# Kernel optimization log

Hardware: AMD Instinct MI355X
Metric: run time of the kernel (lower is better)

The kernel has to match this reference:

```python
import jax, jax.numpy as jnp
import numpy as np

TEMPERATURE = 0.05
BETA = 1.0
LAMBDA_THRESHOLD = 0.7


def setup_inputs() -> dict:
    key = jax.random.key(0)
    k1, k2 = jax.random.split(key)
    B, D = 8192, 256
    features = jax.random.normal(k1, (B, D), dtype=jnp.float32)
    labels = jax.random.randint(k2, (B,), 0, 100, dtype=jnp.int64)
    return {"features": features, "labels": labels}


def reference(features, labels):
    B = features.shape[0]
    eps = 1e-12
    # L2 normalize rows
    f = features / jnp.maximum(jnp.linalg.norm(features, axis=1, keepdims=True), eps)
    sim = jnp.matmul(f, f.T) / TEMPERATURE                      # [B, B]
    sim_max = jnp.max(sim, axis=1, keepdims=True)               # [B, 1]
    sim_stable = sim - sim_max

    same = (labels[:, None] == labels[None, :])
    eye = jnp.eye(B, dtype=bool)
    pos_mask = same & ~eye                                       # [B, B] bool

    # Denominator: logsumexp over all non-self entries per row
    exp_sim = jnp.exp(sim_stable) * (~eye)
    log_denom = jnp.log(jnp.sum(exp_sim, axis=1, keepdims=True) + eps) + sim_max  # [B,1]

    # SCL term: mean over positive pairs of (log_denom[i] - sim[i,j])
    pos_f = pos_mask.astype(sim.dtype)
    n_pos = jnp.sum(pos_f)
    scl_sum = jnp.sum(pos_f * (log_denom - sim))
    scl_loss = jnp.where(n_pos > 0, scl_sum / jnp.maximum(n_pos, 1.0), 0.0)

    # Relaxation term: per row, logsumexp over high-sim positive logits + baseline
    high = (sim * TEMPERATURE > LAMBDA_THRESHOLD) & pos_mask     # [B, B] bool
    neg_inf = jnp.asarray(-jnp.inf, sim.dtype)
    masked_logits = jnp.where(high, sim_stable, neg_inf)          # [B, B]
    baseline = (1.0 / TEMPERATURE) - sim_max                      # [B, 1]
    all_logits = jnp.concatenate([masked_logits, baseline], axis=1)  # [B, B+1]
    row_lse = jax.nn.logsumexp(all_logits, axis=1)                # [B]
    row_has = jnp.any(high, axis=1)
    n_high = jnp.sum(high.astype(sim.dtype))
    relax_sum = jnp.sum(jnp.where(row_has, row_lse, 0.0))
    relaxation_loss = jnp.where(n_high > 0, relax_sum / jnp.maximum(n_high, 1.0), 0.0)

    total = scl_loss + BETA * relaxation_loss
    return jnp.clip(total, 0.0, 10.0)
```

## Files before the change

kernel.cpp:

```cpp
#include <hip/hip_runtime.h>
#include <hip/hip_bf16.h>
#include <math.h>

#define B_N 8192
#define D_K 256
#define TILE 128
#define NT 512
#define NBLK 64
#define NPAIR 2080
#define NCLS 100
#define KEXP 28.8539008177792681f

typedef __attribute__((ext_vector_type(8))) short short8;
typedef __attribute__((ext_vector_type(4))) float f32x4;

__device__ __forceinline__ unsigned short f2bf(float x) {
    unsigned int u = __float_as_uint(x);
    unsigned int r = (u + 0x7FFFu + ((u >> 16) & 1u)) >> 16;
    return (unsigned short)r;
}

__device__ __forceinline__ void gload_lds16(const short* g, short* l) {
    __builtin_amdgcn_global_load_lds(
        (const __attribute__((address_space(1))) void*)g,
        (__attribute__((address_space(3))) void*)l, 16, 0, 0);
}

__device__ __forceinline__ float row_sum16(float v) {
    v += __int_as_float(__builtin_amdgcn_update_dpp(0, __float_as_int(v), 0xB1, 0xF, 0xF, true));
    v += __int_as_float(__builtin_amdgcn_update_dpp(0, __float_as_int(v), 0x4E, 0xF, 0xF, true));
    v += __int_as_float(__builtin_amdgcn_update_dpp(0, __float_as_int(v), 0x141, 0xF, 0xF, true));
    v += __int_as_float(__builtin_amdgcn_update_dpp(0, __float_as_int(v), 0x140, 0xF, 0xF, true));
    return v;
}

__global__ void prep_kernel(const float* __restrict__ feat, unsigned short* __restrict__ fnorm,
                            const int* __restrict__ labels, int* __restrict__ cnt,
                            float* __restrict__ gscal, double* __restrict__ accum,
                            unsigned int* __restrict__ done) {
    if (blockIdx.x == 0) {
        __shared__ int h[NCLS];
        int t = threadIdx.x;
        if (t < NCLS) h[t] = 0;
        if (t == 0) {
            gscal[0] = 0.f; gscal[1] = 0.f;
            accum[0] = 0.0; accum[1] = 0.0; accum[2] = 0.0;
            *done = 0u;
        }
        __syncthreads();
        for (int r = t; r < B_N; r += 256) atomicAdd(&h[labels[r]], 1);
        __syncthreads();
        if (t < NCLS) cnt[t] = h[t];
    }
    int wave = threadIdx.x >> 6, lane = threadIdx.x & 63;
    int row = blockIdx.x * 4 + wave;
    float4 v = *(const float4*)(feat + (size_t)row * D_K + lane * 4);
    float ss = v.x * v.x + v.y * v.y + v.z * v.z + v.w * v.w;
    #pragma unroll
    for (int off = 1; off < 64; off <<= 1) ss += __shfl_xor(ss, off);
    float inv = 1.0f / fmaxf(sqrtf(ss), 1e-12f);
    ushort4 o;
    o.x = f2bf(v.x * inv); o.y = f2bf(v.y * inv);
    o.z = f2bf(v.z * inv); o.w = f2bf(v.w * inv);
    *(ushort4*)(fnorm + (size_t)row * D_K + lane * 4) = o;
}

__global__ __launch_bounds__(NT, 4) void main_kernel(
        const unsigned short* __restrict__ fnorm, const int* __restrict__ labels,
        float2* __restrict__ G, float* __restrict__ gscal) {
    int bid = blockIdx.x;
    int b = (int)((sqrtf(8.0f * bid + 1.0f) - 1.0f) * 0.5f);
    while ((b + 1) * (b + 2) / 2 <= bid) ++b;
    while (b * (b + 1) / 2 > bid) --b;
    int a = bid - b * (b + 1) / 2;
    const int row0 = a * TILE, col0 = b * TILE;
    const bool diag = (a == b);

    __shared__ short As[2][TILE * 64];
    __shared__ short Bs[2][TILE * 64];
    __shared__ int Ls[2 * TILE];
    __shared__ int ghs[8];
    __shared__ float gps[8];

    const int tid = threadIdx.x;
    const int lane = tid & 63, wave = tid >> 6;
    const int wm = wave >> 2, wn = wave & 3;
    const int l15 = lane & 15, lhi = lane >> 4;
    const short* fn = (const short*)fnorm;

    const int id0 = tid, id1 = tid + NT;
    const int r0s = id0 >> 3, c0s = (id0 & 7) ^ (r0s & 7), u0 = (id0 & ~63) * 8;
    const int r1s = id1 >> 3, c1s = (id1 & 7) ^ (r1s & 7), u1 = (id1 & ~63) * 8;

    if (tid < 128) Ls[tid] = labels[row0 + tid];
    else if (tid < 256) Ls[tid] = labels[col0 + tid - 128];
    if (lane == 0) ghs[wave] = 0;

    {
        gload_lds16(fn + (size_t)(row0 + r0s) * D_K + c0s * 8, &As[0][u0]);
        gload_lds16(fn + (size_t)(row0 + r1s) * D_K + c1s * 8, &As[0][u1]);
        if (!diag) {
            gload_lds16(fn + (size_t)(col0 + r0s) * D_K + c0s * 8, &Bs[0][u0]);
            gload_lds16(fn + (size_t)(col0 + r1s) * D_K + c1s * 8, &Bs[0][u1]);
        }
    }

    f32x4 acc[4][2];
    #pragma unroll
    for (int i = 0; i < 4; i++)
        #pragma unroll
        for (int j = 0; j < 2; j++) acc[i][j] = {0.f, 0.f, 0.f, 0.f};

    #pragma unroll
    for (int kc = 0; kc < 4; ++kc) {
        const int cur = kc & 1;
        __syncthreads();
        if (kc < 3) {
            const int nxt = cur ^ 1, ko = (kc + 1) * 64;
            gload_lds16(fn + (size_t)(row0 + r0s) * D_K + ko + c0s * 8, &As[nxt][u0]);
            gload_lds16(fn + (size_t)(row0 + r1s) * D_K + ko + c1s * 8, &As[nxt][u1]);
            if (!diag) {
                gload_lds16(fn + (size_t)(col0 + r0s) * D_K + ko + c0s * 8, &Bs[nxt][u0]);
                gload_lds16(fn + (size_t)(col0 + r1s) * D_K + ko + c1s * 8, &Bs[nxt][u1]);
            }
        }
        const short* Asrc = As[cur];
        const short* Bsrc = diag ? As[cur] : Bs[cur];
        #pragma unroll
        for (int ks = 0; ks < 2; ++ks) {
            short8 af[4], bfr[2];
            #pragma unroll
            for (int mi = 0; mi < 4; mi++) {
                int row = wm * 64 + mi * 16 + l15;
                int ch = (ks * 4 + lhi) ^ (l15 & 7);
                af[mi] = *(const short8*)&Asrc[row * 64 + ch * 8];
            }
            #pragma unroll
            for (int ni = 0; ni < 2; ni++) {
                int row = wn * 32 + ni * 16 + l15;
                int ch = (ks * 4 + lhi) ^ (l15 & 7);
                bfr[ni] = *(const short8*)&Bsrc[row * 64 + ch * 8];
            }
            #pragma unroll
            for (int mi = 0; mi < 4; mi++)
                #pragma unroll
                for (int ni = 0; ni < 2; ni++)
                    acc[mi][ni] = __builtin_amdgcn_mfma_f32_16x16x32_bf16(af[mi], bfr[ni], acc[mi][ni], 0, 0, 0);
        }
    }
    __syncthreads();

    float2* Rbuf = (float2*)As[0];
    float2* Cbuf = (float2*)Bs[0];

    int lc[2], colg[2];
    #pragma unroll
    for (int ni = 0; ni < 2; ni++) {
        int c = wn * 32 + ni * 16 + l15;
        lc[ni] = Ls[128 + c];
        colg[ni] = col0 + c;
    }

    float cD[2] = {0.f, 0.f};
    float gp = 0.f;
    unsigned int hmask = 0;

    #pragma unroll
    for (int mi = 0; mi < 4; mi++) {
        #pragma unroll
        for (int reg = 0; reg < 4; reg++) {
            int rloc = wm * 64 + mi * 16 + lhi * 4 + reg;
            int rowg = row0 + rloc;
            int lr = Ls[rloc];
            float d = 0.f;
            #pragma unroll
            for (int ni = 0; ni < 2; ni++) {
                float dot = acc[mi][ni][reg];
                float e = __builtin_exp2f((dot - 1.0f) * KEXP);
                bool ns = (rowg != colg[ni]);
                float ev = ns ? e : 0.f;
                d += ev; cD[ni] += ev;
                bool ps = ns && (lr == lc[ni]);
                gp += ps ? dot : 0.f;
                bool hi = ps && (dot > 0.7f);
                hmask |= hi ? (1u << ((mi * 4 + reg) * 2 + ni)) : 0u;
            }
            d = row_sum16(d);
            if (l15 == 0) Rbuf[wn * 128 + rloc] = {d, 0.f};
        }
    }

    if (!diag) {
        #pragma unroll
        for (int ni = 0; ni < 2; ni++) {
            cD[ni] += __shfl_xor(cD[ni], 16);
            cD[ni] += __shfl_xor(cD[ni], 32);
        }
        if (lhi == 0) {
            #pragma unroll
            for (int ni = 0; ni < 2; ni++)
                Cbuf[wm * 128 + wn * 32 + ni * 16 + l15] = {cD[ni], 0.f};
        }
    }

    gp = row_sum16(gp);
    gp += __shfl_xor(gp, 16);
    gp += __shfl_xor(gp, 32);
    if (lane == 0) gps[wave] = gp;

    if (__any(hmask != 0)) {
        float cR[2] = {0.f, 0.f};
        #pragma unroll
        for (int mi = 0; mi < 4; mi++) {
            #pragma unroll
            for (int reg = 0; reg < 4; reg++) {
                int rloc = wm * 64 + mi * 16 + lhi * 4 + reg;
                float rx = 0.f;
                #pragma unroll
                for (int ni = 0; ni < 2; ni++) {
                    if (hmask & (1u << ((mi * 4 + reg) * 2 + ni))) {
                        float e = __builtin_exp2f((acc[mi][ni][reg] - 1.0f) * KEXP);
                        rx += e; cR[ni] += e;
                    }
                }
                rx = row_sum16(rx);
                if (l15 == 0) Rbuf[wn * 128 + rloc].y = rx;
            }
        }
        if (!diag) {
            #pragma unroll
            for (int ni = 0; ni < 2; ni++) {
                cR[ni] += __shfl_xor(cR[ni], 16);
                cR[ni] += __shfl_xor(cR[ni], 32);
            }
            if (lhi == 0) {
                #pragma unroll
                for (int ni = 0; ni < 2; ni++)
                    Cbuf[wm * 128 + wn * 32 + ni * 16 + l15].y = cR[ni];
            }
        }
        int nhi = __popc(hmask);
        #pragma unroll
        for (int off = 1; off < 64; off <<= 1) nhi += __shfl_xor(nhi, off);
        if (lane == 0) ghs[wave] = nhi;
    }
    __syncthreads();

    if (tid < 128) {
        int r = tid;
        float2 a0 = Rbuf[r], a1 = Rbuf[128 + r], a2 = Rbuf[256 + r], a3 = Rbuf[384 + r];
        G[(size_t)b * B_N + row0 + r] = {a0.x + a1.x + a2.x + a3.x, a0.y + a1.y + a2.y + a3.y};
    } else if (tid < 256 && !diag) {
        int c = tid - 128;
        float2 a0 = Cbuf[c], a1 = Cbuf[128 + c];
        G[(size_t)a * B_N + col0 + c] = {a0.x + a1.x, a0.y + a1.y};
    }
    if (tid == 0) {
        float w = diag ? 1.0f : 2.0f;
        float gpt = gps[0] + gps[1] + gps[2] + gps[3] + gps[4] + gps[5] + gps[6] + gps[7];
        atomicAdd(&gscal[0], w * gpt);
        int tot = ghs[0] + ghs[1] + ghs[2] + ghs[3] + ghs[4] + ghs[5] + ghs[6] + ghs[7];
        if (tot > 0) atomicAdd(&gscal[1], w * (float)tot);
    }
}

__global__ void finalize_kernel(const float2* __restrict__ G, const int* __restrict__ labels,
                                const int* __restrict__ cnt, const float* __restrict__ gscal,
                                double* __restrict__ accum, unsigned int* __restrict__ done,
                                float* __restrict__ out) {
    int lane = threadIdx.x & 63, q = threadIdx.x >> 6;
    int r = blockIdx.x * 64 + lane;
    float d = 0.f, rx = 0.f;
    #pragma unroll
    for (int s = 0; s < 16; ++s) {
        float2 g = G[(size_t)(q * 16 + s) * B_N + r];
        d += g.x; rx += g.y;
    }
    __shared__ float2 sh[4][64];
    sh[q][lane] = {d, rx};
    __syncthreads();
    if (threadIdx.x < 64) {
        int rr = blockIdx.x * 64 + threadIdx.x;
        float2 t0 = sh[0][threadIdx.x], t1 = sh[1][threadIdx.x];
        float2 t2 = sh[2][threadIdx.x], t3 = sh[3][threadIdx.x];
        float dd = t0.x + t1.x + t2.x + t3.x;
        float rr2 = t0.y + t1.y + t2.y + t3.y;
        float np = (float)(cnt[labels[rr]] - 1);
        float ld = logf(dd + 1e-12f) + 20.0f;
        double s1 = (double)np * (double)ld;
        double s2 = (double)np;
        double s3 = (rr2 > 0.f) ? (double)logf(rr2 + 1.0f) : 0.0;
        #pragma unroll
        for (int off = 1; off < 64; off <<= 1) {
            s1 += __shfl_xor(s1, off);
            s2 += __shfl_xor(s2, off);
            s3 += __shfl_xor(s3, off);
        }
        if (threadIdx.x == 0) {
            atomicAdd(&accum[0], s1);
            atomicAdd(&accum[1], s2);
            atomicAdd(&accum[2], s3);
            __threadfence();
            unsigned int tk = atomicAdd(done, 1u);
            if (tk == gridDim.x - 1) {
                double a1 = atomicAdd(&accum[0], 0.0);
                double a2 = atomicAdd(&accum[1], 0.0);
                double a3 = atomicAdd(&accum[2], 0.0);
                double gp = (double)gscal[0];
                double gh = (double)gscal[1];
                double scl = (a2 > 0.0) ? (a1 - 20.0 * gp) / fmax(a2, 1.0) : 0.0;
                double rel = (gh > 0.0) ? a3 / fmax(gh, 1.0) : 0.0;
                double tot = scl + rel;
                tot = fmin(fmax(tot, 0.0), 10.0);
                out[0] = (float)tot;
            }
        }
    }
}

extern "C" void kernel_launch(void* const* d_in, const int* in_sizes, int n_in,
                              void* d_out, int out_size, void* d_ws, size_t ws_size,
                              hipStream_t stream) {
    const float* feat = (const float*)d_in[0];
    const int* labels = (const int*)d_in[1];
    float* out = (float*)d_out;
    char* ws = (char*)d_ws;

    unsigned short* fnorm = (unsigned short*)(ws);
    float2* G          = (float2*)(ws + (size_t)4 * 1024 * 1024);
    int*    cnt        = (int*)(ws + (size_t)8 * 1024 * 1024);
    float*  gscal      = (float*)(ws + (size_t)8 * 1024 * 1024 + 1024);
    double* accum      = (double*)(ws + (size_t)8 * 1024 * 1024 + 2048);
    unsigned int* done = (unsigned int*)(ws + (size_t)8 * 1024 * 1024 + 3072);

    prep_kernel<<<B_N / 4, 256, 0, stream>>>(feat, fnorm, labels, cnt, gscal, accum, done);
    main_kernel<<<NPAIR, NT, 0, stream>>>(fnorm, labels, G, gscal);
    finalize_kernel<<<B_N / 64, 256, 0, stream>>>(G, labels, cnt, gscal, accum, done, out);
    (void)in_sizes; (void)n_in; (void)out_size; (void)ws_size;
}
```

Before: 120.6 us.

## Halve K-chunk LDS tiles, raise occupancy, template epilogue on diagonal flag

Cuts the per-stage K chunk from 64 to 32 so each double-buffered LDS tile is half the size, with one async global-to-LDS load per thread per stage and precomputed swizzled fragment offsets. Launch bounds go from 4 to 8 blocks per SM to allow more resident blocks. The epilogue is specialised on a compile-time diagonal flag, and the high-similarity bitmask is replaced by recomputing the condition in the second pass. The aim is lower LDS and register pressure and higher occupancy, at the cost of twice as many barrier-separated pipeline stages and a tighter register budget that may cause spills.

```diff
diff --git a/kernel.cpp b/kernel.cpp
--- a/kernel.cpp
+++ b/kernel.cpp
@@ -10,9 +10,13 @@
 #define NPAIR 2080
 #define NCLS 100
 #define KEXP 28.8539008177792681f
+#define KCH 32
+#define NCHUNK 8
 
 typedef __attribute__((ext_vector_type(8))) short short8;
 typedef __attribute__((ext_vector_type(4))) float f32x4;
+
+template <bool V> struct BoolC { static constexpr bool value = V; };
 
 __device__ __forceinline__ unsigned short f2bf(float x) {
     unsigned int u = __float_as_uint(x);
@@ -65,7 +69,7 @@
     *(ushort4*)(fnorm + (size_t)row * D_K + lane * 4) = o;
 }
 
-__global__ __launch_bounds__(NT, 4) void main_kernel(
+__global__ __launch_bounds__(NT, 8) void main_kernel(
         const unsigned short* __restrict__ fnorm, const int* __restrict__ labels,
         float2* __restrict__ G, float* __restrict__ gscal) {
     int bid = blockIdx.x;
@@ -76,8 +80,8 @@
     const int row0 = a * TILE, col0 = b * TILE;
     const bool diag = (a == b);
 
-    __shared__ short As[2][TILE * 64];
-    __shared__ short Bs[2][TILE * 64];
+    __shared__ short As[2][TILE * KCH];
+    __shared__ short Bs[2][TILE * KCH];
     __shared__ int Ls[2 * TILE];
     __shared__ int ghs[8];
     __shared__ float gps[8];
@@ -88,22 +92,17 @@
     const int l15 = lane & 15, lhi = lane >> 4;
     const short* fn = (const short*)fnorm;
 
-    const int id0 = tid, id1 = tid + NT;
-    const int r0s = id0 >> 3, c0s = (id0 & 7) ^ (r0s & 7), u0 = (id0 & ~63) * 8;
-    const int r1s = id1 >> 3, c1s = (id1 & 7) ^ (r1s & 7), u1 = (id1 & ~63) * 8;
+    const int rs = tid >> 2, cs = (tid & 3) ^ (rs & 3);
+    const int uds = (tid & ~63) * 8;
+    const size_t arow = (size_t)(row0 + rs) * D_K + cs * 8;
+    const size_t brow = (size_t)(col0 + rs) * D_K + cs * 8;
 
     if (tid < 128) Ls[tid] = labels[row0 + tid];
     else if (tid < 256) Ls[tid] = labels[col0 + tid - 128];
     if (lane == 0) ghs[wave] = 0;
 
-    {
-        gload_lds16(fn + (size_t)(row0 + r0s) * D_K + c0s * 8, &As[0][u0]);
-        gload_lds16(fn + (size_t)(row0 + r1s) * D_K + c1s * 8, &As[0][u1]);
-        if (!diag) {
-            gload_lds16(fn + (size_t)(col0 + r0s) * D_K + c0s * 8, &Bs[0][u0]);
-            gload_lds16(fn + (size_t)(col0 + r1s) * D_K + c1s * 8, &Bs[0][u1]);
-        }
-    }
+    gload_lds16(fn + arow, &As[0][uds]);
+    if (!diag) gload_lds16(fn + brow, &Bs[0][uds]);
 
     f32x4 acc[4][2];
     #pragma unroll
@@ -111,42 +110,34 @@
         #pragma unroll
         for (int j = 0; j < 2; j++) acc[i][j] = {0.f, 0.f, 0.f, 0.f};
 
-    #pragma unroll
-    for (int kc = 0; kc < 4; ++kc) {
+    const int ch8 = (lhi ^ (l15 & 3)) * 8;
+    int aoff[4], boff[2];
+    #pragma unroll
+    for (int mi = 0; mi < 4; mi++) aoff[mi] = (wm * 64 + mi * 16 + l15) * KCH + ch8;
+    #pragma unroll
+    for (int ni = 0; ni < 2; ni++) boff[ni] = (wn * 32 + ni * 16 + l15) * KCH + ch8;
+
+    #pragma unroll
+    for (int kc = 0; kc < NCHUNK; ++kc) {
         const int cur = kc & 1;
         __syncthreads();
-        if (kc < 3) {
-            const int nxt = cur ^ 1, ko = (kc + 1) * 64;
-            gload_lds16(fn + (size_t)(row0 + r0s) * D_K + ko + c0s * 8, &As[nxt][u0]);
-            gload_lds16(fn + (size_t)(row0 + r1s) * D_K + ko + c1s * 8, &As[nxt][u1]);
-            if (!diag) {
-                gload_lds16(fn + (size_t)(col0 + r0s) * D_K + ko + c0s * 8, &Bs[nxt][u0]);
-                gload_lds16(fn + (size_t)(col0 + r1s) * D_K + ko + c1s * 8, &Bs[nxt][u1]);
-            }
+        if (kc < NCHUNK - 1) {
+            const int nxt = cur ^ 1, ko = (kc + 1) * KCH;
+            gload_lds16(fn + arow + ko, &As[nxt][uds]);
+            if (!diag) gload_lds16(fn + brow + ko, &Bs[nxt][uds]);
         }
         const short* Asrc = As[cur];
         const short* Bsrc = diag ? As[cur] : Bs[cur];
-        #pragma unroll
-        for (int ks = 0; ks < 2; ++ks) {
-            short8 af[4], bfr[2];
-            #pragma unroll
-            for (int mi = 0; mi < 4; mi++) {
-                int row = wm * 64 + mi * 16 + l15;
-                int ch = (ks * 4 + lhi) ^ (l15 & 7);
-                af[mi] = *(const short8*)&Asrc[row * 64 + ch * 8];
-            }
-            #pragma unroll
-            for (int ni = 0; ni < 2; ni++) {
-                int row = wn * 32 + ni * 16 + l15;
-                int ch = (ks * 4 + lhi) ^ (l15 & 7);
-                bfr[ni] = *(const short8*)&Bsrc[row * 64 + ch * 8];
-            }
-            #pragma unroll
-            for (int mi = 0; mi < 4; mi++)
-                #pragma unroll
-                for (int ni = 0; ni < 2; ni++)
-                    acc[mi][ni] = __builtin_amdgcn_mfma_f32_16x16x32_bf16(af[mi], bfr[ni], acc[mi][ni], 0, 0, 0);
-        }
+        short8 af[4], bfr[2];
+        #pragma unroll
+        for (int mi = 0; mi < 4; mi++) af[mi] = *(const short8*)&Asrc[aoff[mi]];
+        #pragma unroll
+        for (int ni = 0; ni < 2; ni++) bfr[ni] = *(const short8*)&Bsrc[boff[ni]];
+        #pragma unroll
+        for (int mi = 0; mi < 4; mi++)
+            #pragma unroll
+            for (int ni = 0; ni < 2; ni++)
+                acc[mi][ni] = __builtin_amdgcn_mfma_f32_16x16x32_bf16(af[mi], bfr[ni], acc[mi][ni], 0, 0, 0);
     }
     __syncthreads();
 
@@ -161,89 +152,96 @@
         colg[ni] = col0 + c;
     }
 
-    float cD[2] = {0.f, 0.f};
-    float gp = 0.f;
-    unsigned int hmask = 0;
-
-    #pragma unroll
-    for (int mi = 0; mi < 4; mi++) {
-        #pragma unroll
-        for (int reg = 0; reg < 4; reg++) {
-            int rloc = wm * 64 + mi * 16 + lhi * 4 + reg;
-            int rowg = row0 + rloc;
-            int lr = Ls[rloc];
-            float d = 0.f;
-            #pragma unroll
-            for (int ni = 0; ni < 2; ni++) {
-                float dot = acc[mi][ni][reg];
-                float e = __builtin_exp2f((dot - 1.0f) * KEXP);
-                bool ns = (rowg != colg[ni]);
-                float ev = ns ? e : 0.f;
-                d += ev; cD[ni] += ev;
-                bool ps = ns && (lr == lc[ni]);
-                gp += ps ? dot : 0.f;
-                bool hi = ps && (dot > 0.7f);
-                hmask |= hi ? (1u << ((mi * 4 + reg) * 2 + ni)) : 0u;
-            }
-            d = row_sum16(d);
-            if (l15 == 0) Rbuf[wn * 128 + rloc] = {d, 0.f};
-        }
-    }
-
-    if (!diag) {
-        #pragma unroll
-        for (int ni = 0; ni < 2; ni++) {
-            cD[ni] += __shfl_xor(cD[ni], 16);
-            cD[ni] += __shfl_xor(cD[ni], 32);
-        }
-        if (lhi == 0) {
-            #pragma unroll
-            for (int ni = 0; ni < 2; ni++)
-                Cbuf[wm * 128 + wn * 32 + ni * 16 + l15] = {cD[ni], 0.f};
-        }
-    }
-
-    gp = row_sum16(gp);
-    gp += __shfl_xor(gp, 16);
-    gp += __shfl_xor(gp, 32);
-    if (lane == 0) gps[wave] = gp;
-
-    if (__any(hmask != 0)) {
-        float cR[2] = {0.f, 0.f};
+    auto body = [&](auto DIAGC) {
+        constexpr bool DIAG = decltype(DIAGC)::value;
+        float cD[2] = {0.f, 0.f};
+        float gp = 0.f;
+        bool anyhi = false;
+
         #pragma unroll
         for (int mi = 0; mi < 4; mi++) {
             #pragma unroll
             for (int reg = 0; reg < 4; reg++) {
                 int rloc = wm * 64 + mi * 16 + lhi * 4 + reg;
-                float rx = 0.f;
+                int rowg = row0 + rloc;
+                int lr = Ls[rloc];
+                float d = 0.f;
                 #pragma unroll
                 for (int ni = 0; ni < 2; ni++) {
-                    if (hmask & (1u << ((mi * 4 + reg) * 2 + ni))) {
-                        float e = __builtin_exp2f((acc[mi][ni][reg] - 1.0f) * KEXP);
-                        rx += e; cR[ni] += e;
-                    }
+                    float dot = acc[mi][ni][reg];
+                    float e = __builtin_exp2f((dot - 1.0f) * KEXP);
+                    bool ns = !DIAG || (rowg != colg[ni]);
+                    float ev = ns ? e : 0.f;
+                    d += ev; cD[ni] += ev;
+                    bool ps = ns && (lr == lc[ni]);
+                    gp += ps ? dot : 0.f;
+                    anyhi = anyhi | (ps & (dot > 0.7f));
                 }
-                rx = row_sum16(rx);
-                if (l15 == 0) Rbuf[wn * 128 + rloc].y = rx;
-            }
-        }
-        if (!diag) {
+                d = row_sum16(d);
+                if (l15 == 0) Rbuf[wn * 128 + rloc] = {d, 0.f};
+            }
+        }
+
+        if (!DIAG) {
             #pragma unroll
             for (int ni = 0; ni < 2; ni++) {
-                cR[ni] += __shfl_xor(cR[ni], 16);
-                cR[ni] += __shfl_xor(cR[ni], 32);
+                cD[ni] += __shfl_xor(cD[ni], 16);
+                cD[ni] += __shfl_xor(cD[ni], 32);
             }
             if (lhi == 0) {
                 #pragma unroll
                 for (int ni = 0; ni < 2; ni++)
-                    Cbuf[wm * 128 + wn * 32 + ni * 16 + l15].y = cR[ni];
-            }
-        }
-        int nhi = __popc(hmask);
-        #pragma unroll
-        for (int off = 1; off < 64; off <<= 1) nhi += __shfl_xor(nhi, off);
-        if (lane == 0) ghs[wave] = nhi;
-    }
+                    Cbuf[wm * 128 + wn * 32 + ni * 16 + l15] = {cD[ni], 0.f};
+            }
+        }
+
+        gp = row_sum16(gp);
+        gp += __shfl_xor(gp, 16);
+        gp += __shfl_xor(gp, 32);
+        if (lane == 0) gps[wave] = gp;
+
+        if (__any(anyhi)) {
+            float cR[2] = {0.f, 0.f};
+            int nhi = 0;
+            #pragma unroll
+            for (int mi = 0; mi < 4; mi++) {
+                #pragma unroll
+                for (int reg = 0; reg < 4; reg++) {
+                    int rloc = wm * 64 + mi * 16 + lhi * 4 + reg;
+                    int rowg = row0 + rloc;
+                    int lr = Ls[rloc];
+                    float rx = 0.f;
+                    #pragma unroll
+                    for (int ni = 0; ni < 2; ni++) {
+                        float dot = acc[mi][ni][reg];
+                        bool ns = !DIAG || (rowg != colg[ni]);
+                        bool hi = ns && (lr == lc[ni]) && (dot > 0.7f);
+                        float e = hi ? __builtin_exp2f((dot - 1.0f) * KEXP) : 0.f;
+                        rx += e; cR[ni] += e; nhi += hi ? 1 : 0;
+                    }
+                    rx = row_sum16(rx);
+                    if (l15 == 0) Rbuf[wn * 128 + rloc].y = rx;
+                }
+            }
+            if (!DIAG) {
+                #pragma unroll
+                for (int ni = 0; ni < 2; ni++) {
+                    cR[ni] += __shfl_xor(cR[ni], 16);
+                    cR[ni] += __shfl_xor(cR[ni], 32);
+                }
+                if (lhi == 0) {
+                    #pragma unroll
+                    for (int ni = 0; ni < 2; ni++)
+                        Cbuf[wm * 128 + wn * 32 + ni * 16 + l15].y = cR[ni];
+                }
+            }
+            #pragma unroll
+            for (int off = 1; off < 64; off <<= 1) nhi += __shfl_xor(nhi, off);
+            if (lane == 0) ghs[wave] = nhi;
+        }
+    };
+    if (diag) body(BoolC<true>{});
+    else body(BoolC<false>{});
     __syncthreads();
 
     if (tid < 128) {
```

New measurement: 173.5 us. 43.8% more time.
